# Kernel tuning notes

Measured on AMD Instinct MI355X. Metric: run time of the kernel, lower is better.

The kernel has to match this reference:

```python
import jax, jax.numpy as jnp
import numpy as np

K = 9  # kernel_size (knn neighbors, loop=True -> self included)

def setup_inputs() -> dict:
    key = jax.random.key(0)
    k1, k2, k3 = jax.random.split(key, 3)
    B, C, H, W = 8, 64, 32, 32
    OUT = 64
    x = jax.random.normal(k1, (B, C, H, W), dtype=jnp.float32)
    # SAGEConv params: lin_l (neighbor aggregate, with bias), lin_r (root, no bias)
    s = 1.0 / np.sqrt(C)
    W_l = jax.random.uniform(k2, (OUT, C), minval=-s, maxval=s, dtype=jnp.float32)
    b_l = jnp.zeros((OUT,), dtype=jnp.float32)
    W_r = jax.random.uniform(k3, (OUT, C), minval=-s, maxval=s, dtype=jnp.float32)
    return {"x": x, "W_l": W_l, "b_l": b_l, "W_r": W_r}

def _knn_mean(x_f, batches):
    # squared-euclidean pairwise distances [N, N], masked across batches
    sq = jnp.sum(x_f * x_f, axis=-1)
    dist = sq[:, None] + sq[None, :] - 2.0 * (x_f @ x_f.T)
    cross = batches[:, None] != batches[None, :]
    dist = jnp.where(cross, jnp.inf, dist)
    neg, idx = jax.lax.top_k(-dist, K)          # k nearest (self included, dist 0)
    valid = (neg != -jnp.inf).astype(x_f.dtype)  # handle degenerate last-batch node
    nbr = x_f[idx] * valid[..., None]            # [N, K, C]
    return nbr.sum(axis=1) / valid.sum(axis=1, keepdims=True)

def reference(x, W_l, b_l, W_r):
    B, C, H, Wd = x.shape
    N = B * H * Wd
    x_f = x.transpose(0, 2, 3, 1).reshape(N, C)  # flat_nodes: [B*H*W, C]
    # torch.linspace(0, B, steps=N).to(int64): truncation of i*B/(N-1)
    batches = jnp.linspace(0.0, float(B), N).astype(jnp.int32)
    mean_nbr = _knn_mean(x_f, batches)
    # SAGEConv: lin_l(mean_j x_j) + lin_r(x_i)
    return mean_nbr @ W_l.T + b_l + x_f @ W_r.T
```

## Files before the change

### kernel.cpp

```cpp
#include <hip/hip_runtime.h>
#include <cstdint>
#include <cstddef>


__global__ __launch_bounds__(256, 2) void k_dist(const float* __restrict__ x,
                                                 const float* __restrict__ Wl,
                                                 const float* __restrict__ Wr,
                                                 const float* __restrict__ bl,
                                                 float* __restrict__ yl,
                                                 float* __restrict__ yr,
                                                 float* __restrict__ D) {
  __shared__ float4 As4[32 * 33];
  __shared__ float4 Bs4[32 * 33];
  __shared__ float sqA[128];
  __shared__ float sqB[128];
  int bx = blockIdx.x, by = blockIdx.y;
  bool is_w = (by >= 64);
  int i0, j0 = 0;
  if (is_w) {
    i0 = (((by - 64) << 3) + bx) << 7;
  } else {
    i0 = by << 7;
    int s = (i0 >= 7168) ? 7168 : (i0 & ~1023);
    j0 = s + (bx << 7);
  }
  const float* xA = x + (((size_t)(i0 >> 10)) << 16) + (i0 & 1023);
  const float* xB = is_w ? xA : x + (((size_t)(j0 >> 10)) << 16) + (j0 & 1023);
  int t = threadIdx.x;
  int tx = t & 15, ty = t >> 4;

  float acc[8][8];
#pragma unroll
  for (int r = 0; r < 8; ++r)
#pragma unroll
    for (int c = 0; c < 8; ++c) acc[r][c] = 0.f;

#pragma unroll 1
  for (int pass = 0; pass < 2; ++pass) {
    if (pass) __syncthreads();
    int c0 = pass << 5;
#pragma unroll
    for (int i = 0; i < 4; ++i) {
      int u = t + (i << 8);
      int c = u >> 5, m4 = u & 31;
      As4[c * 33 + m4] = *(const float4*)&xA[((size_t)(c0 + c) << 10) + (m4 << 2)];
    }
    if (!is_w) {
#pragma unroll
      for (int i = 0; i < 4; ++i) {
        int u = t + (i << 8);
        int c = u >> 5, m4 = u & 31;
        Bs4[c * 33 + m4] = *(const float4*)&xB[((size_t)(c0 + c) << 10) + (m4 << 2)];
      }
    } else {
#pragma unroll
      for (int i = 0; i < 16; ++i) {
        int u = t + (i << 8);
        int j = u >> 5, c = u & 31;
        const float* Wsrc = (j < 64) ? Wl : Wr;
        int jr = j & 63;
        ((float*)&Bs4[c * 33 + (j >> 2)])[j & 3] = Wsrc[(jr << 6) + c0 + c];
      }
    }
    __syncthreads();
    if (!is_w) {
      int m = t & 127;
      const float* base = (t < 128) ? (const float*)As4 : (const float*)Bs4;
      float p = 0.f;
#pragma unroll
      for (int c = 0; c < 32; ++c) {
        float v = base[(c * 33 + (m >> 2)) * 4 + (m & 3)];
        p = fmaf(v, v, p);
      }
      float* dst = (t < 128) ? sqA : sqB;
      if (pass == 0) dst[m] = p; else dst[m] += p;
    }
#pragma unroll 4
    for (int k = 0; k < 32; ++k) {
      float4 a0 = As4[k * 33 + ty];
      float4 a1 = As4[k * 33 + 16 + ty];
      float4 b0 = Bs4[k * 33 + tx];
      float4 b1 = Bs4[k * 33 + 16 + tx];
      float av[8] = {a0.x, a0.y, a0.z, a0.w, a1.x, a1.y, a1.z, a1.w};
      float bv[8] = {b0.x, b0.y, b0.z, b0.w, b1.x, b1.y, b1.z, b1.w};
#pragma unroll
      for (int r = 0; r < 8; ++r)
#pragma unroll
        for (int c = 0; c < 8; ++c)
          acc[r][c] = fmaf(av[r], bv[c], acc[r][c]);
    }
  }
  __syncthreads();

  int rloc[8];
#pragma unroll
  for (int r = 0; r < 4; ++r) { rloc[r] = (ty << 2) + r; rloc[4 + r] = 64 + (ty << 2) + r; }

  if (is_w) {
    float4 blv = *(const float4*)&bl[tx << 2];
#pragma unroll
    for (int r = 0; r < 8; ++r) {
      int n = i0 + rloc[r];
      float4 o0, o1;
      o0.x = acc[r][0]; o0.y = acc[r][1]; o0.z = acc[r][2]; o0.w = acc[r][3];
      o1.x = acc[r][4] + blv.x; o1.y = acc[r][5] + blv.y;
      o1.z = acc[r][6] + blv.z; o1.w = acc[r][7] + blv.w;
      *(float4*)&yl[((size_t)n << 6) + (tx << 2)] = o0;
      *(float4*)&yr[((size_t)n << 6) + (tx << 2)] = o1;
    }
    return;
  }

  int cloc[8];
#pragma unroll
  for (int c = 0; c < 4; ++c) { cloc[c] = (tx << 2) + c; cloc[4 + c] = 64 + (tx << 2) + c; }
  float sqi[8], sqj[8];
#pragma unroll
  for (int r = 0; r < 8; ++r) sqi[r] = sqA[rloc[r]];
#pragma unroll
  for (int c = 0; c < 8; ++c) sqj[c] = sqB[cloc[c]];
#pragma unroll
  for (int r = 0; r < 8; ++r) {
    size_t rb = ((size_t)(i0 + rloc[r]) << 10) + (bx << 7);
    float4 o0, o1;
    o0.x = sqi[r] + sqj[0] - 2.f * acc[r][0];
    o0.y = sqi[r] + sqj[1] - 2.f * acc[r][1];
    o0.z = sqi[r] + sqj[2] - 2.f * acc[r][2];
    o0.w = sqi[r] + sqj[3] - 2.f * acc[r][3];
    o1.x = sqi[r] + sqj[4] - 2.f * acc[r][4];
    o1.y = sqi[r] + sqj[5] - 2.f * acc[r][5];
    o1.z = sqi[r] + sqj[6] - 2.f * acc[r][6];
    o1.w = sqi[r] + sqj[7] - 2.f * acc[r][7];
    *(float4*)&D[rb + (tx << 2)] = o0;
    *(float4*)&D[rb + 64 + (tx << 2)] = o1;
  }
}

__global__ __launch_bounds__(256, 4) void k_selout(const float* __restrict__ D,
                                                   const float* __restrict__ yl,
                                                   const float* __restrict__ yr,
                                                   float* __restrict__ out) {
  int t = threadIdx.x;
  int lane = t & 63;
  int w = t >> 6;
  int n = ((int)blockIdx.x << 2) + w;

  float rv = yr[((size_t)n << 6) + lane];
  float acc;
  if (n == 8191) {
    acc = yl[((size_t)n << 6) + lane];
  } else {
    int s = (n >= 7168) ? 7168 : (n & ~1023);
    bool mlast = (n >= 7168);
    const float* drow = D + ((size_t)n << 10);
    unsigned long long cand[16];
#pragma unroll
    for (int q = 0; q < 4; ++q) {
      float4 v = *(const float4*)&drow[(q << 8) + (lane << 2)];
      float vv[4] = {v.x, v.y, v.z, v.w};
#pragma unroll
      for (int e = 0; e < 4; ++e) {
        unsigned u = __float_as_uint(vv[e]);
        u = (u & 0x80000000u) ? ~u : (u | 0x80000000u);
        unsigned jj = (unsigned)((q << 8) + (lane << 2) + e);
        cand[(q << 2) + e] = ((unsigned long long)u << 32) | jj;
      }
    }
    if (mlast && lane == 63) cand[15] = ~0ull;
    unsigned long long m1 = cand[0], m2 = cand[1];
    if (m2 < m1) { unsigned long long tt = m1; m1 = m2; m2 = tt; }
#pragma unroll
    for (int q = 2; q < 16; ++q) {
      unsigned long long c = cand[q];
      unsigned long long lo = (c < m1) ? c : m1;
      unsigned long long hi = (c < m1) ? m1 : c;
      m2 = (hi < m2) ? hi : m2;
      m1 = lo;
    }
    unsigned long long lm = m1;
    unsigned rmask = 0;
    bool stale = false;
    unsigned j9[9];
#pragma unroll
    for (int kk = 0; kk < 9; ++kk) {
      unsigned long long g = lm;
#pragma unroll
      for (int off = 32; off; off >>= 1) {
        unsigned ghi = __shfl_xor((unsigned)(g >> 32), off, 64);
        unsigned glo = __shfl_xor((unsigned)g, off, 64);
        unsigned long long o = ((unsigned long long)ghi << 32) | glo;
        g = (o < g) ? o : g;
      }
      j9[kk] = (unsigned)s + ((unsigned)g & 1023u);
      if (lm == g) {
        unsigned slot = (((unsigned)g >> 6) & 12u) | ((unsigned)g & 3u);
        rmask |= 1u << slot;
        if (!stale) { lm = m2; stale = true; }
        else {
          unsigned long long best = ~0ull;
#pragma unroll
          for (int q = 0; q < 16; ++q) {
            bool alive = ((rmask >> q) & 1u) == 0u;
            unsigned long long c = cand[q];
            best = (alive && c < best) ? c : best;
          }
          lm = best;
        }
      }
    }
    float g0 = yl[((size_t)j9[0] << 6) + lane];
    float g1 = yl[((size_t)j9[1] << 6) + lane];
    float g2 = yl[((size_t)j9[2] << 6) + lane];
    float g3 = yl[((size_t)j9[3] << 6) + lane];
    float g4 = yl[((size_t)j9[4] << 6) + lane];
    float g5 = yl[((size_t)j9[5] << 6) + lane];
    float g6 = yl[((size_t)j9[6] << 6) + lane];
    float g7 = yl[((size_t)j9[7] << 6) + lane];
    float g8 = yl[((size_t)j9[8] << 6) + lane];
    acc = (((g0 + g1) + (g2 + g3)) + ((g4 + g5) + (g6 + g7)) + g8) * (1.f / 9.f);
  }
  out[((size_t)n << 6) + lane] = acc + rv;
}

extern "C" void kernel_launch(void* const* d_in, const int* in_sizes, int n_in,
                              void* d_out, int out_size, void* d_ws, size_t ws_size,
                              hipStream_t stream) {
  const float* x  = (const float*)d_in[0];
  const float* Wl = (const float*)d_in[1];
  const float* bl = (const float*)d_in[2];
  const float* Wr = (const float*)d_in[3];
  float* out = (float*)d_out;

  char* ws = (char*)d_ws;
  float* yl = (float*)(ws);
  float* yr = (float*)(ws + 2097152);
  float* D  = (float*)(ws + 4194304);

  k_dist<<<dim3(8, 72), 256, 0, stream>>>(x, Wl, Wr, bl, yl, yr, D);
  k_selout<<<2048, 256, 0, stream>>>(D, yl, yr, out);
}
```

Measured before the change: 113.0 us.

## Exploit distance symmetry: compute upper-triangle tiles and write transposed mirror

The distance kernel now computes only the upper-triangular 128x128 tiles within each batch block (36 per batch instead of 64). Each off-diagonal tile's result is also written transposed through shared memory to fill the mirror tile. This roughly halves the GEMM work and input loads for the distance matrix. In exchange it adds an LDS transpose pass with extra syncs, and the output store traffic stays the same. It also uses a 1D grid with a small loop that maps each block index to a triangular tile.

```diff
diff --git a/kernel.cpp b/kernel.cpp
--- a/kernel.cpp
+++ b/kernel.cpp
@@ -10,24 +10,30 @@
                                                  float* __restrict__ yl,
                                                  float* __restrict__ yr,
                                                  float* __restrict__ D) {
-  __shared__ float4 As4[32 * 33];
-  __shared__ float4 Bs4[32 * 33];
+  __shared__ float4 SH[2112];
+  float4* As4 = SH;
+  float4* Bs4 = SH + 1056;
   __shared__ float sqA[128];
   __shared__ float sqB[128];
-  int bx = blockIdx.x, by = blockIdx.y;
-  bool is_w = (by >= 64);
-  int i0, j0 = 0;
+  int bi = (int)blockIdx.x;
+  int t = threadIdx.x;
+  int tx = t & 15, ty = t >> 4;
+
+  bool is_w = (bi >= 288);
+  int i0, j0 = 0, sb = 0, ti = 0, tj = 0;
   if (is_w) {
-    i0 = (((by - 64) << 3) + bx) << 7;
+    i0 = (bi - 288) << 7;
   } else {
-    i0 = by << 7;
-    int s = (i0 >= 7168) ? 7168 : (i0 & ~1023);
-    j0 = s + (bx << 7);
+    int b = bi / 36;
+    int rem = bi - b * 36;
+    while (rem >= 8 - ti) { rem -= (8 - ti); ++ti; }
+    tj = ti + rem;
+    sb = b << 10;
+    i0 = sb + (ti << 7);
+    j0 = sb + (tj << 7);
   }
   const float* xA = x + (((size_t)(i0 >> 10)) << 16) + (i0 & 1023);
   const float* xB = is_w ? xA : x + (((size_t)(j0 >> 10)) << 16) + (j0 & 1023);
-  int t = threadIdx.x;
-  int tx = t & 15, ty = t >> 4;
 
   float acc[8][8];
 #pragma unroll
@@ -120,19 +126,38 @@
 #pragma unroll
   for (int c = 0; c < 8; ++c) sqj[c] = sqB[cloc[c]];
 #pragma unroll
+  for (int r = 0; r < 8; ++r)
+#pragma unroll
+    for (int c = 0; c < 8; ++c)
+      acc[r][c] = sqi[r] + sqj[c] - 2.f * acc[r][c];
+#pragma unroll
   for (int r = 0; r < 8; ++r) {
-    size_t rb = ((size_t)(i0 + rloc[r]) << 10) + (bx << 7);
+    size_t rb = ((size_t)(i0 + rloc[r]) << 10) + (j0 - sb);
     float4 o0, o1;
-    o0.x = sqi[r] + sqj[0] - 2.f * acc[r][0];
-    o0.y = sqi[r] + sqj[1] - 2.f * acc[r][1];
-    o0.z = sqi[r] + sqj[2] - 2.f * acc[r][2];
-    o0.w = sqi[r] + sqj[3] - 2.f * acc[r][3];
-    o1.x = sqi[r] + sqj[4] - 2.f * acc[r][4];
-    o1.y = sqi[r] + sqj[5] - 2.f * acc[r][5];
-    o1.z = sqi[r] + sqj[6] - 2.f * acc[r][6];
-    o1.w = sqi[r] + sqj[7] - 2.f * acc[r][7];
+    o0.x = acc[r][0]; o0.y = acc[r][1]; o0.z = acc[r][2]; o0.w = acc[r][3];
+    o1.x = acc[r][4]; o1.y = acc[r][5]; o1.z = acc[r][6]; o1.w = acc[r][7];
     *(float4*)&D[rb + (tx << 2)] = o0;
     *(float4*)&D[rb + 64 + (tx << 2)] = o1;
+  }
+  if (ti != tj) {
+    float* tb = (float*)SH;
+#pragma unroll 1
+    for (int h = 0; h < 2; ++h) {
+      __syncthreads();
+#pragma unroll
+      for (int r = 0; r < 8; ++r)
+#pragma unroll
+        for (int c = 0; c < 4; ++c)
+          tb[((tx << 2) + c) * 132 + rloc[r]] = acc[r][(h << 2) + c];
+      __syncthreads();
+#pragma unroll
+      for (int it = 0; it < 8; ++it) {
+        int lin = t + (it << 8);
+        int j2 = lin >> 5, u = lin & 31;
+        float4 v = *(const float4*)&tb[j2 * 132 + (u << 2)];
+        *(float4*)&D[((size_t)(j0 + (h << 6) + j2) << 10) + (i0 - sb) + (u << 2)] = v;
+      }
+    }
   }
 }
 
@@ -236,6 +261,6 @@
   float* yr = (float*)(ws + 2097152);
   float* D  = (float*)(ws + 4194304);
 
-  k_dist<<<dim3(8, 72), 256, 0, stream>>>(x, Wl, Wr, bl, yl, yr, D);
+  k_dist<<<dim3(352), 256, 0, stream>>>(x, Wl, Wr, bl, yl, yr, D);
   k_selout<<<2048, 256, 0, stream>>>(D, yl, yr, out);
 }
```

Result: no change. 112.5 us (-0.4%).
